# Kernel tuning notes

Hardware: AMD Instinct MI355X
Metric: run time of the kernel (lower is better)

The kernel has to match this reference:

```python
import jax, jax.numpy as jnp
import numpy as np

B, S, H = 1024, 100, 256          # users(batch), seq_len, hidden
L, U = 20000, 20000               # location_size, user_size
EL, EU = 500000, 400000           # nnz of loc-loc and user-loc sparse graphs
LAMBDA_T, LAMBDA_S = 0.1, 1000.0
DAY = 86400.0


def setup_inputs() -> dict:
    key = jax.random.key(0)
    k = jax.random.split(key, 20)
    sd = 1.0 / np.sqrt(H)
    full_seq = jax.random.randint(k[0], (B, S), 0, L)
    full_seq_map = jax.random.randint(k[1], (B, S), 0, L)
    length = jax.random.randint(k[2], (B,), 1, S + 1)  # >=1 so mask never empty
    user_id = jax.random.randint(k[3], (B,), 0, U)
    time_delta = jax.random.uniform(k[4], (B, S), dtype=jnp.float32) * DAY
    geo_delta = jax.random.uniform(k[5], (B, S), dtype=jnp.float32) * 1e-3
    enc_emb = jax.random.normal(k[6], (L, H), dtype=jnp.float32) * sd
    user_emb = jax.random.normal(k[7], (U, H), dtype=jnp.float32) * sd
    emb2 = jax.random.normal(k[8], (L, H), dtype=jnp.float32) * sd  # embed_layer table
    # loc-loc random-walk graph (row-normalized weights), COO edge list
    row_loc = jax.random.randint(k[9], (EL,), 0, L)
    col_loc = jax.random.randint(k[10], (EL,), 0, L)
    vals_loc = jax.random.uniform(k[11], (EL,), dtype=jnp.float32) / (EL / L)
    # user-loc interact graph (row-normalized), COO edge list
    row_usr = jax.random.randint(k[12], (EU,), 0, U)
    col_usr = jax.random.randint(k[13], (EU,), 0, L)
    vals_usr = jax.random.uniform(k[14], (EU,), dtype=jnp.float32) / (EU / U)
    W_ih = jax.random.normal(k[15], (H, H), dtype=jnp.float32) * sd
    W_hh = jax.random.normal(k[16], (H, H), dtype=jnp.float32) * sd
    b_ih = jnp.zeros((H,), jnp.float32)
    b_hh = jnp.zeros((H,), jnp.float32)
    W1 = jax.random.normal(k[17], (L, 3 * H), dtype=jnp.float32) * sd  # source declares 2H but feeds 3H concat
    b1 = jnp.zeros((L,), jnp.float32)
    h0 = jax.random.normal(k[18], (B, H), dtype=jnp.float32) * (1.0 / H)  # per-user random init state
    return dict(full_seq=full_seq, full_seq_map=full_seq_map, length=length,
                user_id=user_id, time_delta=time_delta, geo_delta=geo_delta,
                enc_emb=enc_emb, user_emb=user_emb, emb2=emb2,
                row_loc=row_loc, col_loc=col_loc, vals_loc=vals_loc,
                row_usr=row_usr, col_usr=col_usr, vals_usr=vals_usr,
                W_ih=W_ih, W_hh=W_hh, b_ih=b_ih, b_hh=b_hh, W1=W1, b1=b1, h0=h0)


def reference(full_seq, full_seq_map, length, user_id, time_delta, geo_delta,
              enc_emb, user_emb, emb2, row_loc, col_loc, vals_loc,
              row_usr, col_usr, vals_usr, W_ih, W_hh, b_ih, b_hh, W1, b1, h0):
    # sparse.mm(graph, loc_emb): one random-walk propagation over locations
    encoder_weight = jax.ops.segment_sum(vals_loc[:, None] * enc_emb[col_loc],
                                         row_loc, num_segments=L)  # [L,H]
    x_emb = encoder_weight[full_seq_map]                           # [B,S,H]
    # sparse.mm(interact_graph, loc_emb): user preference from visited locations
    ew_user = jax.ops.segment_sum(vals_usr[:, None] * enc_emb[col_usr],
                                  row_usr, num_segments=U)         # [U,H]
    user_pref = ew_user[user_id][:, None, :]                       # [B,1,H]
    user_loc_sim = jnp.exp(-jnp.linalg.norm(user_pref - x_emb, axis=-1))  # [B,S]
    # vanilla tanh RNN (batch_first), scan over time
    def step(h, x_t):
        h = jnp.tanh(x_t @ W_ih.T + b_ih + h @ W_hh.T + b_hh)
        return h, h
    _, outs = jax.lax.scan(step, h0, jnp.swapaxes(x_emb, 0, 1))    # [S,B,H]
    out = jnp.swapaxes(outs, 0, 1)                                 # [B,S,H]
    # temporal / spatial decay weights
    a_j = (jnp.cos(time_delta * 2 * np.pi / DAY) + 1) / 2 * jnp.exp(-(time_delta / DAY * LAMBDA_T))
    b_j = jnp.exp(-geo_delta * LAMBDA_S)
    w_j = (a_j * b_j + 1e-10) * user_loc_sim
    mask = (length[:, None] > jnp.arange(S)[None, :]).astype(w_j.dtype)
    w_j = w_j * mask                                               # [B,S]
    denom = jnp.sum(w_j, axis=1, keepdims=True)                    # [B,1]
    out_w = jnp.sum(out * w_j[..., None], axis=1) / denom          # [B,H]
    x2 = emb2[full_seq]                                            # embed_layer (dropout=eval)
    out_w2 = jnp.sum(x2 * w_j[..., None], axis=1) / denom          # [B,H]
    p_u = user_emb[user_id]                                        # [B,H]
    feat = jnp.concatenate([out_w, p_u, out_w2], axis=1)           # [B,3H]
    return feat @ W1.T + b1                                        # [B,L]
```

## Files before the change

kernel.cpp:

```cpp
#include <hip/hip_runtime.h>
#include <math.h>

#define B_  1024
#define S_  100
#define H_  256
#define L_  20000
#define U_  20000
#define EL_ 500000
#define EU_ 400000

typedef __bf16 bf16x8 __attribute__((ext_vector_type(8)));
typedef __bf16 bf16x4 __attribute__((ext_vector_type(4)));
typedef float  f32x4  __attribute__((ext_vector_type(4)));
typedef _Float16 f16x8 __attribute__((ext_vector_type(8)));

__global__ void k_mark(const int* __restrict__ uid, int* __restrict__ flags) {
    int i = blockIdx.x * blockDim.x + threadIdx.x;
    if (i < B_) flags[uid[i]] = 1;
}

__global__ void k_hist2(const int* __restrict__ rowL, const int* __restrict__ rowU,
                        const int* __restrict__ flags,
                        int* __restrict__ cntL, int* __restrict__ cntU) {
    int e = blockIdx.x * blockDim.x + threadIdx.x;
    if (e < EL_) {
        atomicAdd(&cntL[rowL[e]], 1);
    } else if (e < EL_ + EU_) {
        int r = rowU[e - EL_];
        if (flags[r]) atomicAdd(&cntU[r], 1);
    }
}

__global__ __launch_bounds__(1024) void k_scan2(const int* __restrict__ cntA,
                                                int* __restrict__ offsA, int* __restrict__ curA,
                                                const int* __restrict__ cntB,
                                                int* __restrict__ offsB, int* __restrict__ curB) {
    const int* cnt = blockIdx.x ? cntB : cntA;
    int* offs      = blockIdx.x ? offsB : offsA;
    int* cursor    = blockIdx.x ? curB : curA;
    __shared__ int wsum[16];
    __shared__ int carry_s;
    int tid = threadIdx.x;
    int lane = tid & 63, wv = tid >> 6;
    if (tid == 0) carry_s = 0;
    __syncthreads();
    for (int base = 0; base < L_; base += 1024) {
        int v = (base + tid < L_) ? cnt[base + tid] : 0;
        int x = v;
#pragma unroll
        for (int off = 1; off < 64; off <<= 1) {
            int y = __shfl_up(x, off, 64);
            if (lane >= off) x += y;
        }
        if (lane == 63) wsum[wv] = x;
        __syncthreads();
        if (wv == 0) {
            int s = (lane < 16) ? wsum[lane] : 0;
#pragma unroll
            for (int off = 1; off < 16; off <<= 1) {
                int y = __shfl_up(s, off, 64);
                if (lane >= off) s += y;
            }
            if (lane < 16) wsum[lane] = s;
        }
        __syncthreads();
        int excl = x - v + (wv ? wsum[wv - 1] : 0) + carry_s;
        if (base + tid < L_) { offs[base + tid] = excl; cursor[base + tid] = excl; }
        __syncthreads();
        if (tid == 0) carry_s += wsum[15];
        __syncthreads();
    }
    if (tid == 0) offs[L_] = carry_s;
}

__global__ void k_place2(const int* __restrict__ rowL, const int* __restrict__ colL,
                         const float* __restrict__ valL, int* __restrict__ curL,
                         int* __restrict__ colLs, float* __restrict__ valLs,
                         const int* __restrict__ rowU, const int* __restrict__ colU,
                         const float* __restrict__ valU, const int* __restrict__ flags,
                         int* __restrict__ curU, int* __restrict__ colUs,
                         float* __restrict__ valUs) {
    int e = blockIdx.x * blockDim.x + threadIdx.x;
    if (e < EL_) {
        int pos = atomicAdd(&curL[rowL[e]], 1);
        colLs[pos] = colL[e];
        valLs[pos] = valL[e];
    } else if (e < EL_ + EU_) {
        int e2 = e - EL_;
        int r = rowU[e2];
        if (!flags[r]) return;
        int pos = atomicAdd(&curU[r], 1);
        colUs[pos] = colU[e2];
        valUs[pos] = valU[e2];
    }
}

__global__ __launch_bounds__(256) void k_gather2(
        const int* __restrict__ offsL, const int* __restrict__ colLs,
        const float* __restrict__ valLs, float* __restrict__ encw,
        const int* __restrict__ offsU, const int* __restrict__ colUs,
        const float* __restrict__ valUs, float* __restrict__ ewu,
        const int* __restrict__ flags, const float* __restrict__ emb) {
    int r = blockIdx.x;
    const int* offs; const int* col_s; const float* val_s; float* out;
    if (r < L_) {
        offs = offsL; col_s = colLs; val_s = valLs; out = encw;
    } else {
        r -= L_;
        if (!flags[r]) return;
        offs = offsU; col_s = colUs; val_s = valUs; out = ewu;
    }
    int tid = threadIdx.x;
    int lo = offs[r], hi = offs[r + 1];
    float acc = 0.f;
    int i = lo;
    for (; i + 1 < hi; i += 2) {
        int c0 = col_s[i], c1 = col_s[i + 1];
        float v0 = val_s[i], v1 = val_s[i + 1];
        float e0 = emb[(long long)c0 * H_ + tid];
        float e1 = emb[(long long)c1 * H_ + tid];
        acc += v0 * e0 + v1 * e1;
    }
    if (i < hi) acc += val_s[i] * emb[(long long)col_s[i] * H_ + tid];
    out[(long long)r * H_ + tid] = acc;
}

#define BM 128
#define BN 128
#define BK 16
#define PADW 132

__global__ __launch_bounds__(256) void k_gemm(
        const float* __restrict__ A, const float* __restrict__ Bm,
        const float* __restrict__ bias1, const float* __restrict__ bias2,
        float* __restrict__ C, int M, int N, int K) {
    __shared__ float As[BK][PADW];
    __shared__ float Bs[BK][PADW];
    int m0 = blockIdx.x * BM;
    int n0 = blockIdx.y * BN;
    int tid = threadIdx.x;
    int tn = tid & 15, tm = tid >> 4;

    float acc[8][8];
#pragma unroll
    for (int i = 0; i < 8; i++)
#pragma unroll
        for (int j = 0; j < 8; j++) acc[i][j] = 0.f;

    for (int k0 = 0; k0 < K; k0 += BK) {
#pragma unroll
        for (int h = 0; h < 2; h++) {
            int v = tid + h * 256;
            int rw = v >> 2, c4 = v & 3;
            int ar = m0 + rw; if (ar > M - 1) ar = M - 1;
            float4 a = *(const float4*)(A + (long long)ar * K + k0 + c4 * 4);
            As[c4 * 4 + 0][rw] = a.x; As[c4 * 4 + 1][rw] = a.y;
            As[c4 * 4 + 2][rw] = a.z; As[c4 * 4 + 3][rw] = a.w;
            int br = n0 + rw; if (br > N - 1) br = N - 1;
            float4 b = *(const float4*)(Bm + (long long)br * K + k0 + c4 * 4);
            Bs[c4 * 4 + 0][rw] = b.x; Bs[c4 * 4 + 1][rw] = b.y;
            Bs[c4 * 4 + 2][rw] = b.z; Bs[c4 * 4 + 3][rw] = b.w;
        }
        __syncthreads();
#pragma unroll
        for (int kk = 0; kk < BK; kk++) {
            float4 a0 = *(const float4*)&As[kk][tm * 8];
            float4 a1 = *(const float4*)&As[kk][tm * 8 + 4];
            float4 b0 = *(const float4*)&Bs[kk][tn * 8];
            float4 b1 = *(const float4*)&Bs[kk][tn * 8 + 4];
            float av[8] = {a0.x, a0.y, a0.z, a0.w, a1.x, a1.y, a1.z, a1.w};
            float bv[8] = {b0.x, b0.y, b0.z, b0.w, b1.x, b1.y, b1.z, b1.w};
#pragma unroll
            for (int i = 0; i < 8; i++)
#pragma unroll
                for (int j = 0; j < 8; j++) acc[i][j] += av[i] * bv[j];
        }
        __syncthreads();
    }

    float bsum[8];
#pragma unroll
    for (int j = 0; j < 8; j++) {
        int n = n0 + tn * 8 + j;
        float bb = 0.f;
        if (n < N) {
            if (bias1) bb += bias1[n];
            if (bias2) bb += bias2[n];
        }
        bsum[j] = bb;
    }
#pragma unroll
    for (int i = 0; i < 8; i++) {
        int m = m0 + tm * 8 + i;
        if (m < M) {
#pragma unroll
            for (int j = 0; j < 8; j++) {
                int n = n0 + tn * 8 + j;
                if (n < N) C[(long long)m * N + n] = acc[i][j] + bsum[j];
            }
        }
    }
}

__global__ __launch_bounds__(256) void k_cvt(const float4* __restrict__ src,
                                             bf16x4* __restrict__ dst, int n4) {
    int i = blockIdx.x * blockDim.x + threadIdx.x;
    if (i >= n4) return;
    float4 v = src[i];
    bf16x4 o;
    o[0] = (__bf16)v.x; o[1] = (__bf16)v.y; o[2] = (__bf16)v.z; o[3] = (__bf16)v.w;
    dst[i] = o;
}

__global__ __launch_bounds__(256) void k_gemm_bf16(
        const __bf16* __restrict__ A, const __bf16* __restrict__ Bw,
        const float* __restrict__ bias, float* __restrict__ C,
        int M, int N, int K) {
    __shared__ __bf16 Asl[128 * 32];
    __shared__ __bf16 Bsl[128 * 32];
    int tid = threadIdx.x;
    int lane = tid & 63, w = tid >> 6;
    int wm = w >> 1, wn = w & 1;
    int m0 = blockIdx.x * 128, n0 = blockIdx.y * 128;

    f32x4 acc[4][4];
#pragma unroll
    for (int i = 0; i < 4; i++)
#pragma unroll
        for (int j = 0; j < 4; j++) acc[i][j] = (f32x4){0.f, 0.f, 0.f, 0.f};

    int fm = lane & 15, fq = lane >> 4;

    for (int k0 = 0; k0 < K; k0 += 32) {
#pragma unroll
        for (int h = 0; h < 2; h++) {
            int c = h * 256 + w * 64 + lane;
            int r = c >> 2, qsw = c & 3;
            int q = qsw ^ ((r >> 1) & 3);
            const __bf16* gA = A + (long long)(m0 + r) * K + k0 + q * 8;
            __builtin_amdgcn_global_load_lds(
                (const __attribute__((address_space(1))) void*)gA,
                (__attribute__((address_space(3))) void*)(Asl + (h * 256 + w * 64) * 8),
                16, 0, 0);
            int br = n0 + r; if (br > N - 1) br = N - 1;
            const __bf16* gB = Bw + (long long)br * K + k0 + q * 8;
            __builtin_amdgcn_global_load_lds(
                (const __attribute__((address_space(1))) void*)gB,
                (__attribute__((address_space(3))) void*)(Bsl + (h * 256 + w * 64) * 8),
                16, 0, 0);
        }
        __syncthreads();

        bf16x8 af[4], bfr[4];
#pragma unroll
        for (int mi = 0; mi < 4; mi++) {
            int r = wm * 64 + mi * 16 + fm;
            int ch = r * 4 + (fq ^ ((r >> 1) & 3));
            af[mi] = *(const bf16x8*)(Asl + ch * 8);
        }
#pragma unroll
        for (int ni = 0; ni < 4; ni++) {
            int r = wn * 64 + ni * 16 + fm;
            int ch = r * 4 + (fq ^ ((r >> 1) & 3));
            bfr[ni] = *(const bf16x8*)(Bsl + ch * 8);
        }
#pragma unroll
        for (int mi = 0; mi < 4; mi++)
#pragma unroll
            for (int ni = 0; ni < 4; ni++)
                acc[mi][ni] = __builtin_amdgcn_mfma_f32_16x16x32_bf16(
                    af[mi], bfr[ni], acc[mi][ni], 0, 0, 0);
        __syncthreads();
    }

#pragma unroll
    for (int ni = 0; ni < 4; ni++) {
        int col = n0 + wn * 64 + ni * 16 + fm;
        if (col >= N) continue;
        float bb = bias[col];
#pragma unroll
        for (int mi = 0; mi < 4; mi++) {
            int row = m0 + wm * 64 + mi * 16 + fq * 4;
#pragma unroll
            for (int r = 0; r < 4; r++)
                C[(long long)(row + r) * N + col] = acc[mi][ni][r] + bb;
        }
    }
}

__global__ __launch_bounds__(256) void k_simwj(
        const int* __restrict__ map, const int* __restrict__ length, const int* __restrict__ uid,
        const float* __restrict__ td_, const float* __restrict__ gd_,
        const float* __restrict__ encw, const float* __restrict__ ewu,
        float* __restrict__ wj, float* __restrict__ denom) {
    int b = blockIdx.x;
    __shared__ float up[H_];
    __shared__ float wjl[S_];
    int tid = threadIdx.x;
    int u = uid[b];
    up[tid] = ewu[(long long)u * H_ + tid];
    __syncthreads();
    int wv = tid >> 6, lane = tid & 63;
    int len = length[b];
    for (int s = wv; s < S_; s += 4) {
        int mi = map[b * S_ + s];
        float4 x = ((const float4*)(encw + (long long)mi * H_))[lane];
        float4 uu = *(const float4*)&up[lane * 4];
        float dx = uu.x - x.x, dy = uu.y - x.y, dz = uu.z - x.z, dw = uu.w - x.w;
        float d2 = dx * dx + dy * dy + dz * dz + dw * dw;
#pragma unroll
        for (int off = 32; off; off >>= 1) d2 += __shfl_xor(d2, off, 64);
        if (lane == 0) {
            float nrm = sqrtf(d2);
            float sim = expf(-nrm);
            float td = td_[b * S_ + s], gd = gd_[b * S_ + s];
            float aj = (cosf(td * 7.27220521664304e-05f) + 1.0f) * 0.5f *
                       expf(-td * 1.1574074074074073e-06f);
            float bj = expf(-gd * 1000.0f);
            float w = (aj * bj + 1e-10f) * sim;
            if (s >= len) w = 0.f;
            wjl[s] = w;
            wj[b * S_ + s] = w;
        }
    }
    __syncthreads();
    if (tid < 64) {
        float v = (tid < S_) ? wjl[tid] : 0.f;
        if (tid + 64 < S_) v += wjl[tid + 64];
#pragma unroll
        for (int off = 32; off; off >>= 1) v += __shfl_xor(v, off, 64);
        if (tid == 0) denom[b] = v;
    }
}

#define RNN_STRIDE 264

__global__ __launch_bounds__(512, 1) void k_rnn_mfma(
        const float* __restrict__ EWW, const float* __restrict__ Whh,
        const int* __restrict__ map, const float* __restrict__ wj,
        const float* __restrict__ h0g, float* __restrict__ out_acc) {
    __shared__ _Float16 hbuf[2][16 * RNN_STRIDE];
    __shared__ int   maps_s[S_ * 16];
    __shared__ float wjs_s[S_ * 16];

    int tid = threadIdx.x;
    int lane = tid & 63, w = tid >> 6;
    int fm = lane & 15, fq = lane >> 4;
    int b0 = blockIdx.x * 16;

    for (int i = tid; i < 16 * S_; i += 512) {
        int m = i / S_, s = i - m * S_;
        maps_s[s * 16 + m] = map[(b0 + m) * S_ + s];
        wjs_s[s * 16 + m] = wj[(b0 + m) * S_ + s];
    }
    if (tid < 256) {
        int m = tid >> 4, seg = tid & 15;
        const float4* src = (const float4*)(h0g + (long long)(b0 + m) * H_ + seg * 16);
        float4 a = src[0], bq = src[1], cq = src[2], dq = src[3];
        f16x8 v0, v1;
        v0[0] = (_Float16)a.x;  v0[1] = (_Float16)a.y;  v0[2] = (_Float16)a.z;  v0[3] = (_Float16)a.w;
        v0[4] = (_Float16)bq.x; v0[5] = (_Float16)bq.y; v0[6] = (_Float16)bq.z; v0[7] = (_Float16)bq.w;
        v1[0] = (_Float16)cq.x; v1[1] = (_Float16)cq.y; v1[2] = (_Float16)cq.z; v1[3] = (_Float16)cq.w;
        v1[4] = (_Float16)dq.x; v1[5] = (_Float16)dq.y; v1[6] = (_Float16)dq.z; v1[7] = (_Float16)dq.w;
        *(f16x8*)(hbuf[0] + m * RNN_STRIDE + seg * 16) = v0;
        *(f16x8*)(hbuf[0] + m * RNN_STRIDE + seg * 16 + 8) = v1;
    }

    f16x8 wf[2][8];
#pragma unroll
    for (int ni = 0; ni < 2; ni++) {
        const float* wrow = Whh + (long long)(w * 32 + ni * 16 + fm) * H_;
#pragma unroll
        for (int c = 0; c < 8; c++) {
            int k = c * 32 + fq * 8;
            float4 p = *(const float4*)(wrow + k);
            float4 q = *(const float4*)(wrow + k + 4);
            f16x8 v;
            v[0] = (_Float16)p.x; v[1] = (_Float16)p.y; v[2] = (_Float16)p.z; v[3] = (_Float16)p.w;
            v[4] = (_Float16)q.x; v[5] = (_Float16)q.y; v[6] = (_Float16)q.z; v[7] = (_Float16)q.w;
            wf[ni][c] = v;
        }
    }

    float accv[2][4];
#pragma unroll
    for (int ni = 0; ni < 2; ni++)
#pragma unroll
        for (int r = 0; r < 4; r++) accv[ni][r] = 0.f;

    __syncthreads();

    float xc[2][4], xn[2][4];
#pragma unroll
    for (int r = 0; r < 4; r++) {
        const float* xp = EWW + (long long)maps_s[0 * 16 + fq * 4 + r] * H_;
#pragma unroll
        for (int ni = 0; ni < 2; ni++) xc[ni][r] = xp[w * 32 + ni * 16 + fm];
    }

    for (int s = 0; s < S_; s++) {
        const _Float16* hr = hbuf[s & 1];
        _Float16*       hw = hbuf[(s + 1) & 1];

        f32x4 acc[2];
#pragma unroll
        for (int ni = 0; ni < 2; ni++)
            acc[ni] = (f32x4){xc[ni][0], xc[ni][1], xc[ni][2], xc[ni][3]};

        if (s + 1 < S_) {
#pragma unroll
            for (int r = 0; r < 4; r++) {
                const float* xp = EWW + (long long)maps_s[(s + 1) * 16 + fq * 4 + r] * H_;
#pragma unroll
                for (int ni = 0; ni < 2; ni++) xn[ni][r] = xp[w * 32 + ni * 16 + fm];
            }
        }

        f16x8 af[8];
#pragma unroll
        for (int c = 0; c < 8; c++)
            af[c] = *(const f16x8*)(hr + fm * RNN_STRIDE + c * 32 + fq * 8);
#pragma unroll
        for (int c = 0; c < 8; c++)
#pragma unroll
            for (int ni = 0; ni < 2; ni++)
                acc[ni] = __builtin_amdgcn_mfma_f32_16x16x32_f16(af[c], wf[ni][c], acc[ni], 0, 0, 0);

        float wjr[4];
#pragma unroll
        for (int r = 0; r < 4; r++) wjr[r] = wjs_s[s * 16 + fq * 4 + r];
#pragma unroll
        for (int ni = 0; ni < 2; ni++) {
#pragma unroll
            for (int r = 0; r < 4; r++) {
                float t = acc[ni][r];
                t = fminf(15.f, fmaxf(-15.f, t));
                float e = __expf(2.f * t);
                float hv = 1.f - 2.f / (e + 1.f);
                accv[ni][r] += wjr[r] * hv;
                hw[(fq * 4 + r) * RNN_STRIDE + w * 32 + ni * 16 + fm] = (_Float16)hv;
            }
        }

        __syncthreads();

#pragma unroll
        for (int ni = 0; ni < 2; ni++)
#pragma unroll
            for (int r = 0; r < 4; r++) xc[ni][r] = xn[ni][r];
    }

#pragma unroll
    for (int ni = 0; ni < 2; ni++)
#pragma unroll
        for (int r = 0; r < 4; r++)
            out_acc[(long long)(b0 + fq * 4 + r) * H_ + w * 32 + ni * 16 + fm] = accv[ni][r];
}

__global__ __launch_bounds__(256) void k_feat(
        const float* __restrict__ out_acc, const float* __restrict__ denom,
        const int* __restrict__ uid, const float* __restrict__ user_emb,
        const int* __restrict__ seq, const float* __restrict__ wj,
        const float* __restrict__ emb2, float* __restrict__ feat) {
    int b = blockIdx.x, j = threadIdx.x;
    __shared__ float wjl[S_];
    __shared__ int sq[S_];
    if (j < S_) {
        wjl[j] = wj[b * S_ + j];
        sq[j] = seq[b * S_ + j];
    }
    __syncthreads();
    float inv = 1.f / denom[b];
    feat[(long long)b * 768 + j] = out_acc[(long long)b * H_ + j] * inv;
    feat[(long long)b * 768 + 256 + j] = user_emb[(long long)uid[b] * H_ + j];
    float a2 = 0.f;
    for (int s = 0; s < S_; s++) a2 += wjl[s] * emb2[(long long)sq[s] * H_ + j];
    feat[(long long)b * 768 + 512 + j] = a2 * inv;
}

extern "C" void kernel_launch(void* const* d_in, const int* in_sizes, int n_in,
                              void* d_out, int out_size, void* d_ws, size_t ws_size,
                              hipStream_t stream) {
    const int*   full_seq     = (const int*)d_in[0];
    const int*   full_seq_map = (const int*)d_in[1];
    const int*   length       = (const int*)d_in[2];
    const int*   user_id      = (const int*)d_in[3];
    const float* time_delta   = (const float*)d_in[4];
    const float* geo_delta    = (const float*)d_in[5];
    const float* enc_emb      = (const float*)d_in[6];
    const float* user_emb     = (const float*)d_in[7];
    const float* emb2         = (const float*)d_in[8];
    const int*   row_loc      = (const int*)d_in[9];
    const int*   col_loc      = (const int*)d_in[10];
    const float* vals_loc     = (const float*)d_in[11];
    const int*   row_usr      = (const int*)d_in[12];
    const int*   col_usr      = (const int*)d_in[13];
    const float* vals_usr     = (const float*)d_in[14];
    const float* W_ih         = (const float*)d_in[15];
    const float* W_hh         = (const float*)d_in[16];
    const float* b_ih         = (const float*)d_in[17];
    const float* b_hh         = (const float*)d_in[18];
    const float* W1           = (const float*)d_in[19];
    const float* b1           = (const float*)d_in[20];
    const float* h0g          = (const float*)d_in[21];
    float* out = (float*)d_out;

    float* ws = (float*)d_ws;
    size_t o = 0;
    int*   flags = (int*)(ws + o); o += U_;
    float* ewu   = ws + o; o += (size_t)U_ * H_;
    float* encw  = ws + o; o += (size_t)L_ * H_;
    float* EWW   = ws + o; o += (size_t)L_ * H_;
    size_t late_base = o;
    float* wj    = ws + o; o += (size_t)B_ * S_;
    float* denom = ws + o; o += B_;
    float* oacc  = ws + o; o += (size_t)B_ * H_;
    float* feat  = ws + o; o += (size_t)B_ * 3 * H_;
    size_t a = late_base;
    int*   cntL  = (int*)(ws + a); a += L_ + 1;
    int*   offsL = (int*)(ws + a); a += L_ + 1;
    int*   curL  = (int*)(ws + a); a += L_ + 1;
    int*   colLs = (int*)(ws + a); a += EL_;
    float* valLs = ws + a;         a += EL_;
    int*   cntU  = (int*)EWW;
    int*   offsU = cntU + (U_ + 1);
    int*   curU  = offsU + (U_ + 1);
    int*   colUs = curU + (U_ + 1);
    float* valUs = (float*)(colUs + EU_);
    __bf16* w1bf   = (__bf16*)ws;
    __bf16* featbf = (__bf16*)EWW;

    hipMemsetAsync(flags, 0, U_ * sizeof(int), stream);
    hipMemsetAsync(cntL, 0, (L_ + 1) * sizeof(int), stream);
    hipMemsetAsync(cntU, 0, (U_ + 1) * sizeof(int), stream);
    k_mark<<<(B_ + 255) / 256, 256, 0, stream>>>(user_id, flags);

    k_hist2<<<(EL_ + EU_ + 255) / 256, 256, 0, stream>>>(row_loc, row_usr, flags, cntL, cntU);
    k_scan2<<<2, 1024, 0, stream>>>(cntL, offsL, curL, cntU, offsU, curU);
    k_place2<<<(EL_ + EU_ + 255) / 256, 256, 0, stream>>>(
        row_loc, col_loc, vals_loc, curL, colLs, valLs,
        row_usr, col_usr, vals_usr, flags, curU, colUs, valUs);
    k_gather2<<<L_ + U_, 256, 0, stream>>>(offsL, colLs, valLs, encw,
                                           offsU, colUs, valUs, ewu, flags, enc_emb);

    k_gemm<<<dim3((L_ + BM - 1) / BM, (H_ + BN - 1) / BN), 256, 0, stream>>>(
        encw, W_ih, b_ih, b_hh, EWW, L_, H_, H_);
    k_simwj<<<B_, 256, 0, stream>>>(full_seq_map, length, user_id, time_delta,
                                    geo_delta, encw, ewu, wj, denom);
    k_rnn_mfma<<<B_ / 16, 512, 0, stream>>>(EWW, W_hh, full_seq_map, wj, h0g, oacc);
    k_feat<<<B_, 256, 0, stream>>>(oacc, denom, user_id, user_emb, full_seq, wj, emb2, feat);

    k_cvt<<<((L_ * 3 * H_ / 4) + 255) / 256, 256, 0, stream>>>(
        (const float4*)W1, (bf16x4*)w1bf, L_ * 3 * H_ / 4);
    k_cvt<<<((B_ * 3 * H_ / 4) + 255) / 256, 256, 0, stream>>>(
        (const float4*)feat, (bf16x4*)featbf, B_ * 3 * H_ / 4);

    k_gemm_bf16<<<dim3(B_ / 128, (L_ + 127) / 128), 256, 0, stream>>>(
        featbf, w1bf, b1, out, B_, L_, 3 * H_);
}
```

Before: 665.3 us.

## Split RNN hidden columns across 16 waves and fuse bf16 feature conversion

The recurrent kernel now runs 1024 threads (16 waves) per block, with each wave owning 16 hidden columns instead of 32. This halves the serial MFMA chain per wave on every time step and gives more latency hiding per block. The trade-off is more waves taking part in each per-step __syncthreads. Separately, k_feat now writes bf16 features directly, which removes the fp32 feat buffer and one conversion kernel launch.

```diff
diff --git a/kernel.cpp b/kernel.cpp
--- a/kernel.cpp
+++ b/kernel.cpp
@@ -335,7 +335,7 @@
 
 #define RNN_STRIDE 264
 
-__global__ __launch_bounds__(512, 1) void k_rnn_mfma(
+__global__ __launch_bounds__(1024, 1) void k_rnn_mfma(
         const float* __restrict__ EWW, const float* __restrict__ Whh,
         const int* __restrict__ map, const float* __restrict__ wj,
         const float* __restrict__ h0g, float* __restrict__ out_acc) {
@@ -347,8 +347,9 @@
     int lane = tid & 63, w = tid >> 6;
     int fm = lane & 15, fq = lane >> 4;
     int b0 = blockIdx.x * 16;
-
-    for (int i = tid; i < 16 * S_; i += 512) {
+    int col = w * 16 + fm;
+
+    for (int i = tid; i < 16 * S_; i += 1024) {
         int m = i / S_, s = i - m * S_;
         maps_s[s * 16 + m] = map[(b0 + m) * S_ + s];
         wjs_s[s * 16 + m] = wj[(b0 + m) * S_ + s];
@@ -366,10 +367,9 @@
         *(f16x8*)(hbuf[0] + m * RNN_STRIDE + seg * 16 + 8) = v1;
     }
 
-    f16x8 wf[2][8];
-#pragma unroll
-    for (int ni = 0; ni < 2; ni++) {
-        const float* wrow = Whh + (long long)(w * 32 + ni * 16 + fm) * H_;
+    f16x8 wf[8];
+    {
+        const float* wrow = Whh + (long long)col * H_;
 #pragma unroll
         for (int c = 0; c < 8; c++) {
             int k = c * 32 + fq * 8;
@@ -378,42 +378,31 @@
             f16x8 v;
             v[0] = (_Float16)p.x; v[1] = (_Float16)p.y; v[2] = (_Float16)p.z; v[3] = (_Float16)p.w;
             v[4] = (_Float16)q.x; v[5] = (_Float16)q.y; v[6] = (_Float16)q.z; v[7] = (_Float16)q.w;
-            wf[ni][c] = v;
-        }
-    }
-
-    float accv[2][4];
-#pragma unroll
-    for (int ni = 0; ni < 2; ni++)
-#pragma unroll
-        for (int r = 0; r < 4; r++) accv[ni][r] = 0.f;
+            wf[c] = v;
+        }
+    }
+
+    float accv[4];
+#pragma unroll
+    for (int r = 0; r < 4; r++) accv[r] = 0.f;
 
     __syncthreads();
 
-    float xc[2][4], xn[2][4];
-#pragma unroll
-    for (int r = 0; r < 4; r++) {
-        const float* xp = EWW + (long long)maps_s[0 * 16 + fq * 4 + r] * H_;
-#pragma unroll
-        for (int ni = 0; ni < 2; ni++) xc[ni][r] = xp[w * 32 + ni * 16 + fm];
-    }
+    float xc[4], xn[4];
+#pragma unroll
+    for (int r = 0; r < 4; r++)
+        xc[r] = EWW[(long long)maps_s[0 * 16 + fq * 4 + r] * H_ + col];
 
     for (int s = 0; s < S_; s++) {
         const _Float16* hr = hbuf[s & 1];
         _Float16*       hw = hbuf[(s + 1) & 1];
 
-        f32x4 acc[2];
-#pragma unroll
-        for (int ni = 0; ni < 2; ni++)
-            acc[ni] = (f32x4){xc[ni][0], xc[ni][1], xc[ni][2], xc[ni][3]};
+        f32x4 acc = (f32x4){xc[0], xc[1], xc[2], xc[3]};
 
         if (s + 1 < S_) {
 #pragma unroll
-            for (int r = 0; r < 4; r++) {
-                const float* xp = EWW + (long long)maps_s[(s + 1) * 16 + fq * 4 + r] * H_;
-#pragma unroll
-                for (int ni = 0; ni < 2; ni++) xn[ni][r] = xp[w * 32 + ni * 16 + fm];
-            }
+            for (int r = 0; r < 4; r++)
+                xn[r] = EWW[(long long)maps_s[(s + 1) * 16 + fq * 4 + r] * H_ + col];
         }
 
         f16x8 af[8];
@@ -422,46 +411,34 @@
             af[c] = *(const f16x8*)(hr + fm * RNN_STRIDE + c * 32 + fq * 8);
 #pragma unroll
         for (int c = 0; c < 8; c++)
-#pragma unroll
-            for (int ni = 0; ni < 2; ni++)
-                acc[ni] = __builtin_amdgcn_mfma_f32_16x16x32_f16(af[c], wf[ni][c], acc[ni], 0, 0, 0);
-
-        float wjr[4];
-#pragma unroll
-        for (int r = 0; r < 4; r++) wjr[r] = wjs_s[s * 16 + fq * 4 + r];
-#pragma unroll
-        for (int ni = 0; ni < 2; ni++) {
-#pragma unroll
-            for (int r = 0; r < 4; r++) {
-                float t = acc[ni][r];
-                t = fminf(15.f, fmaxf(-15.f, t));
-                float e = __expf(2.f * t);
-                float hv = 1.f - 2.f / (e + 1.f);
-                accv[ni][r] += wjr[r] * hv;
-                hw[(fq * 4 + r) * RNN_STRIDE + w * 32 + ni * 16 + fm] = (_Float16)hv;
-            }
-        }
-
-        __syncthreads();
-
-#pragma unroll
-        for (int ni = 0; ni < 2; ni++)
-#pragma unroll
-            for (int r = 0; r < 4; r++) xc[ni][r] = xn[ni][r];
-    }
-
-#pragma unroll
-    for (int ni = 0; ni < 2; ni++)
-#pragma unroll
-        for (int r = 0; r < 4; r++)
-            out_acc[(long long)(b0 + fq * 4 + r) * H_ + w * 32 + ni * 16 + fm] = accv[ni][r];
+            acc = __builtin_amdgcn_mfma_f32_16x16x32_f16(af[c], wf[c], acc, 0, 0, 0);
+
+#pragma unroll
+        for (int r = 0; r < 4; r++) {
+            float t = acc[r];
+            t = fminf(15.f, fmaxf(-15.f, t));
+            float e = __expf(2.f * t);
+            float hv = 1.f - 2.f / (e + 1.f);
+            accv[r] += wjs_s[s * 16 + fq * 4 + r] * hv;
+            hw[(fq * 4 + r) * RNN_STRIDE + col] = (_Float16)hv;
+        }
+
+        __syncthreads();
+
+#pragma unroll
+        for (int r = 0; r < 4; r++) xc[r] = xn[r];
+    }
+
+#pragma unroll
+    for (int r = 0; r < 4; r++)
+        out_acc[(long long)(b0 + fq * 4 + r) * H_ + col] = accv[r];
 }
 
 __global__ __launch_bounds__(256) void k_feat(
         const float* __restrict__ out_acc, const float* __restrict__ denom,
         const int* __restrict__ uid, const float* __restrict__ user_emb,
         const int* __restrict__ seq, const float* __restrict__ wj,
-        const float* __restrict__ emb2, float* __restrict__ feat) {
+        const float* __restrict__ emb2, __bf16* __restrict__ featb) {
     int b = blockIdx.x, j = threadIdx.x;
     __shared__ float wjl[S_];
     __shared__ int sq[S_];
@@ -471,11 +448,11 @@
     }
     __syncthreads();
     float inv = 1.f / denom[b];
-    feat[(long long)b * 768 + j] = out_acc[(long long)b * H_ + j] * inv;
-    feat[(long long)b * 768 + 256 + j] = user_emb[(long long)uid[b] * H_ + j];
+    featb[(long long)b * 768 + j] = (__bf16)(out_acc[(long long)b * H_ + j] * inv);
+    featb[(long long)b * 768 + 256 + j] = (__bf16)(user_emb[(long long)uid[b] * H_ + j]);
     float a2 = 0.f;
     for (int s = 0; s < S_; s++) a2 += wjl[s] * emb2[(long long)sq[s] * H_ + j];
-    feat[(long long)b * 768 + 512 + j] = a2 * inv;
+    featb[(long long)b * 768 + 512 + j] = (__bf16)(a2 * inv);
 }
 
 extern "C" void kernel_launch(void* const* d_in, const int* in_sizes, int n_in,
@@ -515,8 +492,7 @@
     float* wj    = ws + o; o += (size_t)B_ * S_;
     float* denom = ws + o; o += B_;
     float* oacc  = ws + o; o += (size_t)B_ * H_;
-    float* feat  = ws + o; o += (size_t)B_ * 3 * H_;
-    size_t a = late_base;
+    size_t a = o;
     int*   cntL  = (int*)(ws + a); a += L_ + 1;
     int*   offsL = (int*)(ws + a); a += L_ + 1;
     int*   curL  = (int*)(ws + a); a += L_ + 1;
@@ -547,13 +523,11 @@
         encw, W_ih, b_ih, b_hh, EWW, L_, H_, H_);
     k_simwj<<<B_, 256, 0, stream>>>(full_seq_map, length, user_id, time_delta,
                                     geo_delta, encw, ewu, wj, denom);
-    k_rnn_mfma<<<B_ / 16, 512, 0, stream>>>(EWW, W_hh, full_seq_map, wj, h0g, oacc);
-    k_feat<<<B_, 256, 0, stream>>>(oacc, denom, user_id, user_emb, full_seq, wj, emb2, feat);
+    k_rnn_mfma<<<B_ / 16, 1024, 0, stream>>>(EWW, W_hh, full_seq_map, wj, h0g, oacc);
+    k_feat<<<B_, 256, 0, stream>>>(oacc, denom, user_id, user_emb, full_seq, wj, emb2, featbf);
 
     k_cvt<<<((L_ * 3 * H_ / 4) + 255) / 256, 256, 0, stream>>>(
         (const float4*)W1, (bf16x4*)w1bf, L_ * 3 * H_ / 4);
-    k_cvt<<<((B_ * 3 * H_ / 4) + 255) / 256, 256, 0, stream>>>(
-        (const float4*)feat, (bf16x4*)featbf, B_ * 3 * H_ / 4);
 
     k_gemm_bf16<<<dim3(B_ / 128, (L_ + 127) / 128), 256, 0, stream>>>(
         featbf, w1bf, b1, out, B_, L_, 3 * H_);
```

After: 654.7 us. No clear change (-1.6%).
